# Performance work log

Hardware: AMD Instinct MI355X
Metric: run time of the kernel (lower is better)

Reference implementation:

```python
import jax, jax.numpy as jnp
import numpy as np

# Module hyperparameters (from init_kwargs)
L = 32        # spatial length
CIN = 128     # in_channels
COUT = 256    # out_channels
N = 8         # num_filters
STRIDE = 1
K = 9         # kernel_size (l//4+1 default for l>16)


def setup_inputs() -> dict:
    key = jax.random.key(0)
    kx, kw = jax.random.split(key)
    x = jax.random.normal(kx, (32, CIN, L, L), dtype=jnp.float32)
    # weight init: uniform in [-r, r], r = sqrt(1/(cin*k*k)), shape (n, cin//8, k, k)
    r = np.sqrt(1.0 / (CIN * K * K)).astype(np.float32)
    weight = (jax.random.uniform(kw, (N, CIN // 8, K, K), dtype=jnp.float32) - 0.5) * 2.0 * r
    return {"x": x, "weight": weight}


def reference(x, weight):
    # 3D real FFT over (channel, H, W) of the input: [B, CIN, L, L//2+1] complex
    x_hat = jnp.fft.rfftn(x, axes=(1, 2, 3))
    # Zero-pad weight (cin//8 -> CIN, k -> L) and transform: [N, CIN, L, L//2+1]
    w_hat = jnp.fft.rfftn(weight, s=(CIN, L, L))
    # Broadcast multiply (no channel reduction): [B, N, CIN, L, L//2+1]
    freq_out = jnp.einsum('bchw,nchw->bnchw', x_hat, w_hat)
    # Inverse 3D real FFT over (channel, H, W): [B, N, CIN, L, L]
    out = jnp.fft.irfftn(freq_out, axes=(2, 3, 4))
    # Channel shrink: keep every shrink_ratio-th channel -> CIN/shrink = COUT/N channels
    shrink_ratio = N * CIN // COUT
    out = out[:, :, ::shrink_ratio]                       # [B, N, COUT//N, L, L]
    out = out.reshape(out.shape[0], -1, out.shape[3], out.shape[4])  # [B, COUT, L, L]
    if STRIDE == 2:
        out = out[:, :, ::2, ::2]
    return out
```

## Files before the change

### kernel.cpp

```cpp
#include <hip/hip_runtime.h>

typedef __attribute__((ext_vector_type(4)))  float f32x4;
typedef __attribute__((ext_vector_type(16))) float f32x16;
typedef __attribute__((ext_vector_type(8)))  short s16x8;

#define KK 9
#define NCHUNK 23

__device__ inline unsigned short f2bf(float f) {
    union { float f; unsigned int u; } v; v.f = f;
    unsigned int u = v.u + 0x7FFFu + ((v.u >> 16) & 1u);
    return (unsigned short)(u >> 16);
}


__global__ void prep_w32(const float* __restrict__ wgt, unsigned short* __restrict__ Bg) {
    int idx = blockIdx.x * 256 + threadIdx.x;
    if (idx >= 108 * 64 * 8) return;
    int e     = idx & 7;
    int lanei = (idx >> 3) & 63;
    int chunk = idx >> 9;
    int col   = lanei & 31;
    int khalf = lanei >> 5;
    int n  = col & 7;
    int p  = col >> 3;
    int kx = chunk / 12;
    int s  = chunk - 12 * kx;
    int ky = s - 3 + p;
    int cp = khalf * 8 + e;
    int dc = 15 - cp;
    float val = 0.f;
    if (ky >= 0 && ky <= 8)
        val = wgt[((n * 16 + dc) * KK + ky) * KK + kx];
    Bg[idx] = f2bf(val);
}

__global__ __launch_bounds__(512, 8) void fconv_mfma32(
    const float* __restrict__ x,
    const unsigned short* __restrict__ Bg,
    float* __restrict__ out)
{
    __shared__ char smb[32768];

    const int tid = threadIdx.x;
    const int b   = blockIdx.x >> 5;
    const int j   = blockIdx.x & 31;

    const float* xb = x + ((size_t)b << 17);
    int choff[16];
    #pragma unroll
    for (int i = 0; i < 16; ++i)
        choff[i] = ((4 * j - 15 + i) & 127) << 10;

    #pragma unroll
    for (int i = 0; i < 2; ++i) {
        int cell = i * 512 + tid;
        #pragma unroll
        for (int h = 0; h < 2; ++h) {
            union { unsigned short u16[8]; uint4 v; } pk;
            #pragma unroll
            for (int e = 0; e < 8; ++e)
                pk.u16[e] = f2bf(xb[choff[h * 8 + e] + cell]);
            *(uint4*)(smb + h * 16384 + cell * 16) = pk.v;
        }
    }
    __syncthreads();

    const int lane  = tid & 63;
    const int wave  = tid >> 6;
    const int wrow  = lane & 31;
    const int khalf = lane >> 5;
    const int g4    = wave * 4;

    f32x16 acc = (f32x16)0.f;
    const char* bp = (const char*)Bg + (lane << 4);

    #pragma unroll 1
    for (int kx = 0; kx < 9; ++kx) {
        const int abase = (khalf << 14) + (((wrow - kx) & 31) << 4);
        const char* bpk = bp + ((kx * 12) << 10);
        #pragma unroll
        for (int s = 0; s < 12; ++s) {
            int yp = (g4 + 3 - s) & 31;
            s16x8 a  = *(const s16x8*)(smb + abase + (yp << 9));
            s16x8 bb = *(const s16x8*)(bpk + (s << 10));
            acc = __builtin_amdgcn_mfma_f32_32x32x16_bf16(a, bb, acc, 0, 0, 0);
        }
    }

    const int n = wrow & 7;
    const int p = wrow >> 3;
    float* ob = out + (((size_t)(b * 256 + n * 32 + j)) << 10)
                    + ((g4 + p) << 5) + 4 * khalf;
    #pragma unroll
    for (int q = 0; q < 4; ++q) {
        f32x4 v = { acc[4*q], acc[4*q+1], acc[4*q+2], acc[4*q+3] };
        *(f32x4*)(ob + q * 8) = v;
    }
}

__global__ void prep_w(const float* __restrict__ wgt, unsigned short* __restrict__ Bg) {
    int idx = blockIdx.x * 256 + threadIdx.x;
    if (idx >= NCHUNK * 4 * 16 * 8) return;
    int e   = idx & 7;
    int col = (idx >> 3) & 15;
    int g   = (idx >> 7) & 3;
    int c   = idx >> 9;
    int pi   = g >> 1;
    int half = g & 1;
    int cp = half * 8 + e;
    int dc = 15 - cp;
    int q  = 2 * c + pi;
    int n  = col & 7;
    int t  = col >> 3;
    float val = 0.f;
    if (q <= 44) {
        int ky2 = q / 9;
        int kx  = q - 9 * ky2;
        int ky  = 2 * ky2 + t;
        if (ky <= 8)
            val = wgt[((n * 16 + dc) * KK + ky) * KK + kx];
    }
    Bg[idx] = f2bf(val);
}

__global__ __launch_bounds__(256) void fconv_mfma(
    const float* __restrict__ x,
    const unsigned short* __restrict__ Bg,
    float* __restrict__ out)
{
    __shared__ char smem[32768 + 4096];
    char*  smb     = smem;
    float* handoff = (float*)(smem + 32768);

    const int tid = threadIdx.x;
    const int b   = blockIdx.x >> 5;
    const int j   = blockIdx.x & 31;

    const float* xb = x + ((size_t)b << 17);
    int choff[16];
    #pragma unroll
    for (int i = 0; i < 16; ++i)
        choff[i] = ((4 * j - 15 + i) & 127) << 10;

    #pragma unroll
    for (int i = 0; i < 4; ++i) {
        int cell = i * 256 + tid;
        #pragma unroll
        for (int h = 0; h < 2; ++h) {
            union { unsigned short u16[8]; uint4 v; } pk;
            #pragma unroll
            for (int e = 0; e < 8; ++e)
                pk.u16[e] = f2bf(xb[choff[h * 8 + e] + cell]);
            *(uint4*)(smb + h * 16384 + cell * 16) = pk.v;
        }
    }
    __syncthreads();

    const int lane = tid & 63;
    const int wave = tid >> 6;
    const int r    = lane & 15;
    const int g    = lane >> 4;
    const int half = g & 1;
    const int pi   = g >> 1;
    const int y0   = wave * 8;

    f32x4 acc[8][2];
    #pragma unroll
    for (int dy = 0; dy < 8; ++dy) { acc[dy][0] = (f32x4)0.f; acc[dy][1] = (f32x4)0.f; }

    const char* bptr = (const char*)Bg + ((g * 16 + r) << 4);
    s16x8 bfrag = *(const s16x8*)(bptr);

    #pragma unroll 1
    for (int c = 0; c < NCHUNK; ++c) {
        int q   = 2 * c + pi;
        int ky2 = q / 9;
        int kx  = q - 9 * ky2;
        int wr  = (r - kx) & 31;
        int yb  = (y0 - 2 * ky2) & 31;
        int abase = (half << 14) + (wr << 4);

        int cn = (c < NCHUNK - 1) ? c + 1 : NCHUNK - 1;
        s16x8 bnext = *(const s16x8*)(bptr + (cn << 10));

        #pragma unroll
        for (int dy = 0; dy < 8; ++dy) {
            int yy = (yb + dy) & 31;
            int ra = abase + (yy << 9);
            s16x8 a0 = *(const s16x8*)(smb + ra);
            s16x8 a1 = *(const s16x8*)(smb + (ra ^ 256));
            acc[dy][0] = __builtin_amdgcn_mfma_f32_16x16x32_bf16(a0, bfrag, acc[dy][0], 0, 0, 0);
            acc[dy][1] = __builtin_amdgcn_mfma_f32_16x16x32_bf16(a1, bfrag, acc[dy][1], 0, 0, 0);
        }
        bfrag = bnext;
    }

    float recv[8][2][4];
    #pragma unroll
    for (int dy = 0; dy < 8; ++dy)
        #pragma unroll
        for (int h = 0; h < 2; ++h)
            #pragma unroll
            for (int i = 0; i < 4; ++i)
                recv[dy][h][i] = __shfl_xor(acc[dy][h][i], 8);

    if (r < 8) {
        #pragma unroll
        for (int h = 0; h < 2; ++h)
            *(f32x4*)&handoff[wave * 256 + r * 32 + h * 16 + g * 4] = *(f32x4*)recv[7][h];
    }
    __syncthreads();

    if (r < 8) {
        const int pw = (wave + 3) & 3;
        f32x4 prev[2];
        #pragma unroll
        for (int h = 0; h < 2; ++h)
            prev[h] = *(f32x4*)&handoff[pw * 256 + r * 32 + h * 16 + g * 4];

        float* ob = out + (((size_t)(b * 256 + r * 32 + j)) << 10) + (g << 2);
        #pragma unroll
        for (int dy = 0; dy < 8; ++dy) {
            #pragma unroll
            for (int h = 0; h < 2; ++h) {
                f32x4 t1 = (dy == 0) ? prev[h] : *(f32x4*)recv[dy - 1][h];
                f32x4 v  = acc[dy][h] + t1;
                *(f32x4*)(ob + (y0 + dy) * 32 + h * 16) = v;
            }
        }
    }
}

__global__ __launch_bounds__(256, 2) void fconv_fallback(
    const float* __restrict__ x,
    const float* __restrict__ wgt,
    float* __restrict__ out)
{
    __shared__ float sw[16 * KK * KK * 8];
    const int tid = threadIdx.x;
    for (int idx = tid; idx < 8 * 16 * KK * KK; idx += 256) {
        int n  = idx / (16 * KK * KK);
        int rm = idx - n * (16 * KK * KK);
        int dc = rm / (KK * KK);
        int r2 = rm - dc * (KK * KK);
        int ky = r2 / KK;
        int kx = r2 - ky * KK;
        sw[((dc * KK + kx) * KK + ky) * 8 + n] = wgt[idx];
    }
    __syncthreads();

    const int bid = blockIdx.x;
    const int b   = bid >> 6;
    const int j   = (bid >> 1) & 31;
    const int yh  = bid & 1;
    const int xw  = tid & 31;
    const int yg  = tid >> 5;
    const int y_base = yh * 16 + yg * 2;

    int rows[10];
    #pragma unroll
    for (int i = 0; i < 10; ++i)
        rows[i] = ((y_base + 24 + i) & 31) << 5;

    float acc[8][2];
    #pragma unroll
    for (int n = 0; n < 8; ++n) { acc[n][0] = 0.f; acc[n][1] = 0.f; }

    const int c0 = 4 * j;
    #pragma unroll 1
    for (int dc = 0; dc < 16; ++dc) {
        const int c_src = (c0 - dc) & 127;
        const float* bx = x + (((size_t)b * 128 + c_src) << 10);
        #pragma unroll 1
        for (int kx = 0; kx < KK; ++kx) {
            const int x_col = (xw - kx) & 31;
            float win[10];
            #pragma unroll
            for (int i = 0; i < 10; ++i)
                win[i] = bx[rows[i] + x_col];
            const float4* wp = (const float4*)&sw[((dc * KK + kx) * KK) * 8];
            #pragma unroll
            for (int ky = 0; ky < KK; ++ky) {
                float4 wA = wp[2 * ky];
                float4 wB = wp[2 * ky + 1];
                float x0 = win[8 - ky];
                float x1 = win[9 - ky];
                acc[0][0] += x0 * wA.x; acc[0][1] += x1 * wA.x;
                acc[1][0] += x0 * wA.y; acc[1][1] += x1 * wA.y;
                acc[2][0] += x0 * wA.z; acc[2][1] += x1 * wA.z;
                acc[3][0] += x0 * wA.w; acc[3][1] += x1 * wA.w;
                acc[4][0] += x0 * wB.x; acc[4][1] += x1 * wB.x;
                acc[5][0] += x0 * wB.y; acc[5][1] += x1 * wB.y;
                acc[6][0] += x0 * wB.z; acc[6][1] += x1 * wB.z;
                acc[7][0] += x0 * wB.w; acc[7][1] += x1 * wB.w;
            }
        }
    }
    #pragma unroll
    for (int n = 0; n < 8; ++n) {
        float* op = out + ((((size_t)b * 256) + n * 32 + j) << 10) + (y_base << 5) + xw;
        op[0]  = acc[n][0];
        op[32] = acc[n][1];
    }
}

extern "C" void kernel_launch(void* const* d_in, const int* in_sizes, int n_in,
                              void* d_out, int out_size, void* d_ws, size_t ws_size,
                              hipStream_t stream) {
    const float* x   = (const float*)d_in[0];
    const float* w   = (const float*)d_in[1];
    float*       out = (float*)d_out;

    const size_t BG32_BYTES = (size_t)108 * 64 * 8 * sizeof(unsigned short);
    const size_t BG16_BYTES = (size_t)NCHUNK * 4 * 16 * 8 * sizeof(unsigned short);

    if (ws_size >= BG32_BYTES) {
        unsigned short* Bg = (unsigned short*)d_ws;
        prep_w32<<<216, 256, 0, stream>>>(w, Bg);
        fconv_mfma32<<<1024, 512, 0, stream>>>(x, Bg, out);
    } else if (ws_size >= BG16_BYTES) {
        unsigned short* Bg = (unsigned short*)d_ws;
        prep_w<<<46, 256, 0, stream>>>(w, Bg);
        fconv_mfma<<<1024, 256, 0, stream>>>(x, Bg, out);
    } else {
        fconv_fallback<<<2048, 256, 0, stream>>>(x, w, out);
    }
}
```

Before: 113.0 us.

## Process two output channel groups per block to reuse weight fragments

Each block now computes two channel-offset positions (j and j+16) instead of one, staging both input slices into a doubled shared-memory buffer and keeping two accumulators. The weight B fragments for each kx are loaded once into registers and used for both MFMA streams, halving global weight loads per MFMA and giving the matrix unit two independent chains. The cost is doubled LDS per block, lower occupancy (launch bounds 4, grid halved to 512 blocks) and more register pressure.

New measurement: 106.9 us. 1.06x faster.

```diff
diff --git a/kernel.cpp b/kernel.cpp
--- a/kernel.cpp
+++ b/kernel.cpp
@@ -35,33 +35,37 @@
     Bg[idx] = f2bf(val);
 }
 
-__global__ __launch_bounds__(512, 8) void fconv_mfma32(
+__global__ __launch_bounds__(512, 4) void fconv_mfma32(
     const float* __restrict__ x,
     const unsigned short* __restrict__ Bg,
     float* __restrict__ out)
 {
-    __shared__ char smb[32768];
+    __shared__ char smb[65536];
 
     const int tid = threadIdx.x;
-    const int b   = blockIdx.x >> 5;
-    const int j   = blockIdx.x & 31;
+    const int b   = blockIdx.x >> 4;
+    const int jp  = blockIdx.x & 15;
 
     const float* xb = x + ((size_t)b << 17);
-    int choff[16];
-    #pragma unroll
-    for (int i = 0; i < 16; ++i)
-        choff[i] = ((4 * j - 15 + i) & 127) << 10;
-
-    #pragma unroll
-    for (int i = 0; i < 2; ++i) {
-        int cell = i * 512 + tid;
-        #pragma unroll
-        for (int h = 0; h < 2; ++h) {
-            union { unsigned short u16[8]; uint4 v; } pk;
-            #pragma unroll
-            for (int e = 0; e < 8; ++e)
-                pk.u16[e] = f2bf(xb[choff[h * 8 + e] + cell]);
-            *(uint4*)(smb + h * 16384 + cell * 16) = pk.v;
+    #pragma unroll
+    for (int t = 0; t < 2; ++t) {
+        const int j = jp + t * 16;
+        int choff[16];
+        #pragma unroll
+        for (int i = 0; i < 16; ++i)
+            choff[i] = ((4 * j - 15 + i) & 127) << 10;
+
+        #pragma unroll
+        for (int i = 0; i < 2; ++i) {
+            int cell = i * 512 + tid;
+            #pragma unroll
+            for (int h = 0; h < 2; ++h) {
+                union { unsigned short u16[8]; uint4 v; } pk;
+                #pragma unroll
+                for (int e = 0; e < 8; ++e)
+                    pk.u16[e] = f2bf(xb[choff[h * 8 + e] + cell]);
+                *(uint4*)(smb + t * 32768 + h * 16384 + cell * 16) = pk.v;
+            }
         }
     }
     __syncthreads();
@@ -72,30 +76,50 @@
     const int khalf = lane >> 5;
     const int g4    = wave * 4;
 
-    f32x16 acc = (f32x16)0.f;
+    f32x16 acc0 = (f32x16)0.f;
+    f32x16 acc1 = (f32x16)0.f;
     const char* bp = (const char*)Bg + (lane << 4);
 
     #pragma unroll 1
     for (int kx = 0; kx < 9; ++kx) {
         const int abase = (khalf << 14) + (((wrow - kx) & 31) << 4);
-        const char* bpk = bp + ((kx * 12) << 10);
+        const char* bpk = bp + kx * 12288;
+
+        s16x8 bb[12];
+        #pragma unroll
+        for (int s = 0; s < 12; ++s)
+            bb[s] = *(const s16x8*)(bpk + (s << 10));
+
         #pragma unroll
         for (int s = 0; s < 12; ++s) {
             int yp = (g4 + 3 - s) & 31;
-            s16x8 a  = *(const s16x8*)(smb + abase + (yp << 9));
-            s16x8 bb = *(const s16x8*)(bpk + (s << 10));
-            acc = __builtin_amdgcn_mfma_f32_32x32x16_bf16(a, bb, acc, 0, 0, 0);
+            const char* ap = smb + abase + (yp << 9);
+            s16x8 a0 = *(const s16x8*)(ap);
+            s16x8 a1 = *(const s16x8*)(ap + 32768);
+            acc0 = __builtin_amdgcn_mfma_f32_32x32x16_bf16(a0, bb[s], acc0, 0, 0, 0);
+            acc1 = __builtin_amdgcn_mfma_f32_32x32x16_bf16(a1, bb[s], acc1, 0, 0, 0);
         }
     }
 
     const int n = wrow & 7;
     const int p = wrow >> 3;
-    float* ob = out + (((size_t)(b * 256 + n * 32 + j)) << 10)
-                    + ((g4 + p) << 5) + 4 * khalf;
-    #pragma unroll
-    for (int q = 0; q < 4; ++q) {
-        f32x4 v = { acc[4*q], acc[4*q+1], acc[4*q+2], acc[4*q+3] };
-        *(f32x4*)(ob + q * 8) = v;
+    {
+        float* ob = out + (((size_t)(b * 256 + n * 32 + jp)) << 10)
+                        + ((g4 + p) << 5) + 4 * khalf;
+        #pragma unroll
+        for (int q = 0; q < 4; ++q) {
+            f32x4 v = { acc0[4*q], acc0[4*q+1], acc0[4*q+2], acc0[4*q+3] };
+            *(f32x4*)(ob + q * 8) = v;
+        }
+    }
+    {
+        float* ob = out + (((size_t)(b * 256 + n * 32 + jp + 16)) << 10)
+                        + ((g4 + p) << 5) + 4 * khalf;
+        #pragma unroll
+        for (int q = 0; q < 4; ++q) {
+            f32x4 v = { acc1[4*q], acc1[4*q+1], acc1[4*q+2], acc1[4*q+3] };
+            *(f32x4*)(ob + q * 8) = v;
+        }
     }
 }
 
@@ -318,7 +342,7 @@
     if (ws_size >= BG32_BYTES) {
         unsigned short* Bg = (unsigned short*)d_ws;
         prep_w32<<<216, 256, 0, stream>>>(w, Bg);
-        fconv_mfma32<<<1024, 512, 0, stream>>>(x, Bg, out);
+        fconv_mfma32<<<512, 512, 0, stream>>>(x, Bg, out);
     } else if (ws_size >= BG16_BYTES) {
         unsigned short* Bg = (unsigned short*)d_ws;
         prep_w<<<46, 256, 0, stream>>>(w, Bg);
```
